# Optimization experiments

Hardware: AMD Instinct MI355X
Metric: run time of the kernel (lower is better)

The kernel has to match this reference:

```python
import jax, jax.numpy as jnp
import numpy as np

MASK_VAL = -10000.0
HEADS = 16

def setup_inputs() -> dict:
    key = jax.random.key(0)
    ks = jax.random.split(key, 4)
    dim = 1024
    x = jax.random.normal(ks[0], (4, 2048, dim), dtype=jnp.float32)
    Wq = jax.random.normal(ks[1], (dim, dim), dtype=jnp.float32) * (dim ** -0.5)
    Wkv = jax.random.normal(ks[2], (dim, 2 * dim), dtype=jnp.float32) * (dim ** -0.5)
    Wout = jax.random.normal(ks[3], (dim, dim), dtype=jnp.float32) * (dim ** -0.5)
    bout = jnp.zeros((dim,), dtype=jnp.float32)
    return {"x": x, "Wq": Wq, "Wkv": Wkv, "Wout": Wout, "bout": bout}

def reference(x, Wq, Wkv, Wout, bout):
    b, n, dim = x.shape
    h = HEADS
    d = dim // h
    scale = dim ** -0.5  # NOTE: module scales by full dim, not head dim
    q = x @ Wq                       # [b,n,dim]
    kv = x @ Wkv                     # [b,n,2*dim]
    k, v = jnp.split(kv, 2, axis=-1)
    split = lambda t: t.reshape(b, n, h, d).transpose(0, 2, 1, 3)  # b h n d
    q, k, v = split(q), split(k), split(v)
    dots = jnp.einsum('bhid,bhjd->bhij', q, k) * scale
    causal = jnp.triu(jnp.ones((n, n), dtype=bool), 1)
    dots = jnp.where(causal, MASK_VAL, dots)
    attn = jax.nn.softmax(dots, axis=-1)
    out = jnp.einsum('bhij,bhjd->bhid', attn, v)
    out = out.transpose(0, 2, 1, 3).reshape(b, n, dim)
    return out @ Wout + bout
```

## Files before the change

kernel.cpp:

```cpp
#include <hip/hip_runtime.h>

typedef unsigned short u16;
typedef __attribute__((ext_vector_type(4))) float f32x4;
typedef __attribute__((ext_vector_type(8))) short bf16x8;

#define MFMA_BF16(a, b, c) __builtin_amdgcn_mfma_f32_16x16x32_bf16((a), (b), (c), 0, 0, 0)

static constexpr int kDim   = 1024;
static constexpr int kSeq   = 2048;
static constexpr int kBatch = 4;
static constexpr int kHeads = 16;
static constexpr int kTok   = kBatch * kSeq;
static constexpr int kQKV   = 3 * kDim;
static constexpr float kQscale = 0.045084220027780106f;

__device__ __forceinline__ u16 f2bf(float f) {
  unsigned int u = __float_as_uint(f);
  u += 0x7fffu + ((u >> 16) & 1u);
  return (u16)(u >> 16);
}

__device__ __forceinline__ float fast_exp2(float x) {
#if __has_builtin(__builtin_amdgcn_exp2f)
  return __builtin_amdgcn_exp2f(x);
#else
  return exp2f(x);
#endif
}

__device__ __forceinline__ unsigned pack_bf16(float lo, float hi) {
  const unsigned ulo = __float_as_uint(lo) + 0x8000u;
  const unsigned uhi = __float_as_uint(hi) + 0x8000u;
#if __has_builtin(__builtin_amdgcn_perm)
  return __builtin_amdgcn_perm(uhi, ulo, 0x07060302u);
#else
  return (uhi & 0xFFFF0000u) | (ulo >> 16);
#endif
}

__device__ __forceinline__ void gl_lds16(const void* g, void* l) {
  __builtin_amdgcn_global_load_lds(
      (const __attribute__((address_space(1))) void*)g,
      (__attribute__((address_space(3))) void*)l, 16, 0, 0);
}

__global__ __launch_bounds__(256) void cvt_f32_to_bf16(const float* __restrict__ in,
                                                       u16* __restrict__ out, int n8) {
  int i = blockIdx.x * 256 + threadIdx.x;
  if (i >= n8) return;
  const float4* p = (const float4*)in + (size_t)i * 2;
  float4 a = p[0], b = p[1];
  alignas(16) u16 o[8];
  o[0] = f2bf(a.x); o[1] = f2bf(a.y); o[2] = f2bf(a.z); o[3] = f2bf(a.w);
  o[4] = f2bf(b.x); o[5] = f2bf(b.y); o[6] = f2bf(b.z); o[7] = f2bf(b.w);
  *(uint4*)(out + (size_t)i * 8) = *(const uint4*)o;
}

__global__ __launch_bounds__(256) void transpose_cvt(const float* __restrict__ src,
                                                     u16* __restrict__ dst, int R, int C) {
  __shared__ u16 tile[64][65];
  const int r0 = blockIdx.y * 64, c0 = blockIdx.x * 64;
  const int t = threadIdx.x;
#pragma unroll
  for (int i = 0; i < 16; ++i) {
    const int idx = i * 256 + t;
    const int rr = idx >> 6, cc = idx & 63;
    tile[rr][cc] = f2bf(src[(size_t)(r0 + rr) * C + c0 + cc]);
  }
  __syncthreads();
#pragma unroll
  for (int i = 0; i < 16; ++i) {
    const int idx = i * 256 + t;
    const int rr = idx >> 6, cc = idx & 63;
    dst[(size_t)(c0 + rr) * R + r0 + cc] = tile[cc][rr];
  }
}

__global__ __launch_bounds__(256) void transpose_v(const u16* __restrict__ QKV,
                                                   u16* __restrict__ Vt) {
  __shared__ u16 tile[64][65];
  const int n0 = blockIdx.x * 64;
  const int bh = blockIdx.y;
  const int b = bh >> 4, h = bh & 15;
  const int t = threadIdx.x;
#pragma unroll
  for (int i = 0; i < 16; ++i) {
    const int idx = i * 256 + t;
    const int nn = idx >> 6, dd = idx & 63;
    tile[nn][dd] = QKV[(size_t)(b * kSeq + n0 + nn) * kQKV + 2048 + h * 64 + dd];
  }
  __syncthreads();
#pragma unroll
  for (int i = 0; i < 16; ++i) {
    const int idx = i * 256 + t;
    const int dd = idx >> 6, nn = idx & 63;
    Vt[((size_t)bh * 64 + dd) * kSeq + n0 + nn] = tile[nn][dd];
  }
}

template <int OUT_F32>
__global__ __launch_bounds__(256) void gemm_bt(const u16* __restrict__ A,
                                               const u16* __restrict__ Bt,
                                               void* __restrict__ Cout,
                                               const float* __restrict__ bias,
                                               int M, int N, int K,
                                               int qcols, float qs) {
  __shared__ u16 As[128 * 32];
  __shared__ u16 Bs[128 * 32];
  const int t = threadIdx.x;
  const int l = t & 63, w = t >> 6;
  const int g = l >> 4, r = l & 15;

  const int gx = gridDim.x;
  int wg = blockIdx.y * gx + blockIdx.x;
  const int chunk = (gx * gridDim.y) >> 3;
  wg = (wg & 7) * chunk + (wg >> 3);
  const int m0 = (wg / gx) * 128, n0 = (wg % gx) * 128;
  const int wr = (w >> 1) * 64, wc = (w & 1) * 64;

  f32x4 acc[4][4];
#pragma unroll
  for (int m = 0; m < 4; ++m)
#pragma unroll
    for (int n = 0; n < 4; ++n) acc[m][n] = f32x4{0.f, 0.f, 0.f, 0.f};

  const int rowi = t >> 2;
  const int coli = (t & 3) * 8;
  const u16* ga = A + (size_t)(m0 + rowi) * K + coli;
  const u16* gb = Bt + (size_t)(n0 + rowi) * K + coli;
  char* lA = (char*)As + t * 16;
  char* lB = (char*)Bs + t * 16;

  for (int k0 = 0; k0 < K; k0 += 32) {
    gl_lds16(ga + k0, lA);
    gl_lds16(ga + k0 + (size_t)64 * K, lA + 4096);
    gl_lds16(gb + k0, lB);
    gl_lds16(gb + k0 + (size_t)64 * K, lB + 4096);
    __syncthreads();
    bf16x8 af[4], bfr[4];
#pragma unroll
    for (int m = 0; m < 4; ++m)
      af[m] = *(const bf16x8*)(As + (wr + m * 16 + r) * 32 + g * 8);
#pragma unroll
    for (int n = 0; n < 4; ++n)
      bfr[n] = *(const bf16x8*)(Bs + (wc + n * 16 + r) * 32 + g * 8);
#pragma unroll
    for (int m = 0; m < 4; ++m)
#pragma unroll
      for (int n = 0; n < 4; ++n)
        acc[m][n] = MFMA_BF16(af[m], bfr[n], acc[m][n]);
    __syncthreads();
  }

#pragma unroll
  for (int m = 0; m < 4; ++m)
#pragma unroll
    for (int n = 0; n < 4; ++n)
#pragma unroll
      for (int j = 0; j < 4; ++j) {
        const int row = m0 + wr + m * 16 + g * 4 + j;
        const int col = n0 + wc + n * 16 + r;
        if (OUT_F32) {
          ((float*)Cout)[(size_t)row * N + col] = acc[m][n][j] + bias[col];
        } else {
          float v = acc[m][n][j];
          if (col < qcols) v *= qs;
          ((u16*)Cout)[(size_t)row * N + col] = f2bf(v);
        }
      }
}

__global__ __launch_bounds__(512, 4) void attn_fwd(const u16* __restrict__ QKV,
                                                   const u16* __restrict__ Vt,
                                                   u16* __restrict__ Ob) {
  __shared__ u16 Kl[64 * 64];
  __shared__ u16 Vl[64 * 64];
  int wg = blockIdx.y * 8 + blockIdx.x;
  wg = (wg & 7) * 64 + (wg >> 3);
  const int ib = wg & 7;
  const int bh = wg >> 3;
  const int b = bh >> 4, h = bh & 15;
  const int t = threadIdx.x;
  const int w = t >> 6;
  const int l = t & 63;
  const int g = l >> 4;
  const int qr = l & 15;
  const int sw = qr & 7;
  const int srow = t >> 3;
  const int sgran = t & 7;
  const int sg_off = (sgran ^ (srow & 7)) * 8;

  const u16* kbase = QKV + (size_t)b * kSeq * kQKV + 1024 + h * 64 + (size_t)srow * kQKV + sg_off;
  const u16* vbase = Vt + ((size_t)bh * 64 + srow) * kSeq + sg_off;

  for (int pass = 0; pass < 2; ++pass) {
    const int qblk = pass ? (15 - ib) : ib;
    const int q0 = qblk * 128;
    const int qrow_g = q0 + w * 16 + qr;

    const u16* qptr = QKV + (size_t)(b * kSeq + qrow_g) * kQKV + h * 64 + g * 8;
    bf16x8 qf[2];
    qf[0] = *(const bf16x8*)qptr;
    qf[1] = *(const bf16x8*)(qptr + 32);

    f32x4 oacc[4];
#pragma unroll
    for (int d = 0; d < 4; ++d) oacc[d] = f32x4{0.f, 0.f, 0.f, 0.f};
    float lsum = 0.f;

    const int nkv = 2 * qblk + 2;
    for (int kb = 0; kb < nkv; ++kb) {
      const int kv0 = kb * 64;
      gl_lds16(kbase + (size_t)kv0 * kQKV, (char*)Kl + t * 16);
      gl_lds16(vbase + kv0, (char*)Vl + t * 16);
      __syncthreads();

      const bool any_valid = kv0 <= q0 + w * 16 + 15;
      const bool need_mask = kv0 + 63 > q0 + w * 16;

      if (any_valid) {
        f32x4 sacc[4];
#pragma unroll
        for (int n = 0; n < 4; ++n) sacc[n] = f32x4{0.f, 0.f, 0.f, 0.f};
        __builtin_amdgcn_s_setprio(1);
#pragma unroll
        for (int n = 0; n < 4; ++n)
#pragma unroll
          for (int c = 0; c < 2; ++c) {
            bf16x8 kf = *(const bf16x8*)(Kl + (n * 16 + qr) * 64 + ((c * 4 + g) ^ sw) * 8);
            sacc[n] = MFMA_BF16(kf, qf[c], sacc[n]);
          }
        __builtin_amdgcn_s_setprio(0);

        float s2[16];
#pragma unroll
        for (int n = 0; n < 4; ++n)
#pragma unroll
          for (int j = 0; j < 4; ++j) s2[n * 4 + j] = sacc[n][j];
        if (need_mask) {
#pragma unroll
          for (int n = 0; n < 4; ++n)
#pragma unroll
            for (int j = 0; j < 4; ++j) {
              const int kv = kv0 + n * 16 + g * 4 + j;
              if (kv > qrow_g) s2[n * 4 + j] = -30000.0f;
            }
        }

        unsigned pk[4][2];
#pragma unroll
        for (int n = 0; n < 4; ++n)
#pragma unroll
          for (int hw = 0; hw < 2; ++hw) {
            const float p0 = fast_exp2(fminf(s2[n * 4 + hw * 2], 60.f));
            const float p1 = fast_exp2(fminf(s2[n * 4 + hw * 2 + 1], 60.f));
            lsum += p0 + p1;
            pk[n][hw] = pack_bf16(p0, p1);
          }

        const int src0 = qr | (((g << 1) & 3) << 4);
        const int src1 = qr | ((((g << 1) + 1) & 3) << 4);
        const bool hi = (g >> 1) != 0;
#pragma unroll
        for (int c = 0; c < 2; ++c) {
          const unsigned a0 = __shfl(pk[2 * c][0], src0);
          const unsigned a1 = __shfl(pk[2 * c][1], src0);
          const unsigned a2 = __shfl(pk[2 * c + 1][0], src0);
          const unsigned a3 = __shfl(pk[2 * c + 1][1], src0);
          const unsigned b0 = __shfl(pk[2 * c][0], src1);
          const unsigned b1 = __shfl(pk[2 * c][1], src1);
          const unsigned b2 = __shfl(pk[2 * c + 1][0], src1);
          const unsigned b3 = __shfl(pk[2 * c + 1][1], src1);
          union { unsigned u[4]; bf16x8 v; } af;
          af.u[0] = hi ? a2 : a0;
          af.u[1] = hi ? a3 : a1;
          af.u[2] = hi ? b2 : b0;
          af.u[3] = hi ? b3 : b1;
          __builtin_amdgcn_s_setprio(1);
#pragma unroll
          for (int d = 0; d < 4; ++d) {
            bf16x8 vf = *(const bf16x8*)(Vl + (d * 16 + qr) * 64 + ((c * 4 + g) ^ sw) * 8);
            oacc[d] = MFMA_BF16(af.v, vf, oacc[d]);
          }
          __builtin_amdgcn_s_setprio(0);
        }
      }
      __syncthreads();
    }

    lsum += __shfl_xor(lsum, 16);
    lsum += __shfl_xor(lsum, 32);
    const float invl = 1.0f / lsum;
    float ir[4];
#pragma unroll
    for (int j = 0; j < 4; ++j) ir[j] = __shfl(invl, (l & 48) | (g * 4 + j));
#pragma unroll
    for (int d = 0; d < 4; ++d)
#pragma unroll
      for (int j = 0; j < 4; ++j) {
        const int row = q0 + w * 16 + g * 4 + j;
        const int col = h * 64 + d * 16 + qr;
        Ob[(size_t)(b * kSeq + row) * kDim + col] = f2bf(oacc[d][j] * ir[j]);
      }
  }
}

extern "C" void kernel_launch(void* const* d_in, const int* in_sizes, int n_in,
                              void* d_out, int out_size, void* d_ws, size_t ws_size,
                              hipStream_t stream) {
  const float* x    = (const float*)d_in[0];
  const float* Wq   = (const float*)d_in[1];
  const float* Wkv  = (const float*)d_in[2];
  const float* Wout = (const float*)d_in[3];
  const float* bout = (const float*)d_in[4];
  float* out = (float*)d_out;

  char* p = (char*)d_ws;
  u16* xb    = (u16*)p; p += (size_t)kTok * kDim * 2;
  u16* Wqkvt = (u16*)p; p += (size_t)kQKV * kDim * 2;
  u16* Wot   = (u16*)p; p += (size_t)kDim * kDim * 2;
  u16* QKV   = (u16*)p; p += (size_t)kTok * kQKV * 2;
  u16* Vt    = (u16*)p; p += (size_t)64 * 64 * kSeq * 2;
  u16* Ob    = (u16*)p; p += (size_t)kTok * kDim * 2;

  const int n8 = kTok * kDim / 8;
  cvt_f32_to_bf16<<<dim3((n8 + 255) / 256), 256, 0, stream>>>(x, xb, n8);
  transpose_cvt<<<dim3(kDim / 64, kDim / 64), 256, 0, stream>>>(Wq, Wqkvt, kDim, kDim);
  transpose_cvt<<<dim3(2 * kDim / 64, kDim / 64), 256, 0, stream>>>(
      Wkv, Wqkvt + (size_t)kDim * kDim, kDim, 2 * kDim);
  transpose_cvt<<<dim3(kDim / 64, kDim / 64), 256, 0, stream>>>(Wout, Wot, kDim, kDim);

  gemm_bt<0><<<dim3(kQKV / 128, kTok / 128), 256, 0, stream>>>(
      xb, Wqkvt, QKV, nullptr, kTok, kQKV, kDim, kDim, kQscale);
  transpose_v<<<dim3(kSeq / 64, kBatch * kHeads), 256, 0, stream>>>(QKV, Vt);
  attn_fwd<<<dim3(kSeq / 256, kBatch * kHeads), 512, 0, stream>>>(QKV, Vt, Ob);
  gemm_bt<1><<<dim3(kDim / 128, kTok / 128), 256, 0, stream>>>(
      Ob, Wot, out, bout, kTok, kDim, kDim, 0, 1.0f);
}
```

Measured before the change: 274.4 us.

## Double-buffer K/V tiles in attention and widen GEMM K-step with swizzled LDS

In the attention kernel, K and V tiles are now double-buffered in shared memory. The next tile's global-to-LDS load is issued before computing on the current one, with explicit vmcnt waits and raw barriers, so load latency overlaps the MFMA and softmax work. In the projection GEMM, the K step grows from 32 to 64 and LDS tiles use an XOR swizzle, which halves the barrier count and is meant to avoid bank conflicts. The cost is double the LDS per block, which may lower occupancy, and a dependence on hand-written waitcnt ordering for correctness.

```diff
diff --git a/kernel.cpp b/kernel.cpp
--- a/kernel.cpp
+++ b/kernel.cpp
@@ -105,8 +105,8 @@
                                                const float* __restrict__ bias,
                                                int M, int N, int K,
                                                int qcols, float qs) {
-  __shared__ u16 As[128 * 32];
-  __shared__ u16 Bs[128 * 32];
+  __shared__ u16 As[128 * 64];
+  __shared__ u16 Bs[128 * 64];
   const int t = threadIdx.x;
   const int l = t & 63, w = t >> 6;
   const int g = l >> 4, r = l & 15;
@@ -124,31 +124,37 @@
 #pragma unroll
     for (int n = 0; n < 4; ++n) acc[m][n] = f32x4{0.f, 0.f, 0.f, 0.f};
 
-  const int rowi = t >> 2;
-  const int coli = (t & 3) * 8;
-  const u16* ga = A + (size_t)(m0 + rowi) * K + coli;
-  const u16* gb = Bt + (size_t)(n0 + rowi) * K + coli;
+  const int srow = t >> 3;
+  const int sgran = t & 7;
+  const int scol = (sgran ^ (srow & 7)) * 8;
+  const u16* ga = A + (size_t)(m0 + srow) * K + scol;
+  const u16* gb = Bt + (size_t)(n0 + srow) * K + scol;
   char* lA = (char*)As + t * 16;
   char* lB = (char*)Bs + t * 16;
-
-  for (int k0 = 0; k0 < K; k0 += 32) {
-    gl_lds16(ga + k0, lA);
-    gl_lds16(ga + k0 + (size_t)64 * K, lA + 4096);
-    gl_lds16(gb + k0, lB);
-    gl_lds16(gb + k0 + (size_t)64 * K, lB + 4096);
+  const int rsw = r & 7;
+
+  for (int k0 = 0; k0 < K; k0 += 64) {
+#pragma unroll
+    for (int i = 0; i < 4; ++i) {
+      gl_lds16(ga + k0 + (size_t)(i * 32) * K, lA + i * 4096);
+      gl_lds16(gb + k0 + (size_t)(i * 32) * K, lB + i * 4096);
+    }
     __syncthreads();
-    bf16x8 af[4], bfr[4];
-#pragma unroll
-    for (int m = 0; m < 4; ++m)
-      af[m] = *(const bf16x8*)(As + (wr + m * 16 + r) * 32 + g * 8);
-#pragma unroll
-    for (int n = 0; n < 4; ++n)
-      bfr[n] = *(const bf16x8*)(Bs + (wc + n * 16 + r) * 32 + g * 8);
-#pragma unroll
-    for (int m = 0; m < 4; ++m)
+#pragma unroll
+    for (int kk = 0; kk < 2; ++kk) {
+      bf16x8 af[4], bfr[4];
+#pragma unroll
+      for (int m = 0; m < 4; ++m)
+        af[m] = *(const bf16x8*)(As + (wr + m * 16 + r) * 64 + (((kk * 4 + g) ^ rsw) * 8));
 #pragma unroll
       for (int n = 0; n < 4; ++n)
-        acc[m][n] = MFMA_BF16(af[m], bfr[n], acc[m][n]);
+        bfr[n] = *(const bf16x8*)(Bs + (wc + n * 16 + r) * 64 + (((kk * 4 + g) ^ rsw) * 8));
+#pragma unroll
+      for (int m = 0; m < 4; ++m)
+#pragma unroll
+        for (int n = 0; n < 4; ++n)
+          acc[m][n] = MFMA_BF16(af[m], bfr[n], acc[m][n]);
+    }
     __syncthreads();
   }
 
@@ -173,8 +179,8 @@
 __global__ __launch_bounds__(512, 4) void attn_fwd(const u16* __restrict__ QKV,
                                                    const u16* __restrict__ Vt,
                                                    u16* __restrict__ Ob) {
-  __shared__ u16 Kl[64 * 64];
-  __shared__ u16 Vl[64 * 64];
+  __shared__ u16 Kl[2][64 * 64];
+  __shared__ u16 Vl[2][64 * 64];
   int wg = blockIdx.y * 8 + blockIdx.x;
   wg = (wg & 7) * 64 + (wg >> 3);
   const int ib = wg & 7;
@@ -209,12 +215,26 @@
     float lsum = 0.f;
 
     const int nkv = 2 * qblk + 2;
+
+    gl_lds16(kbase, (char*)Kl[0] + t * 16);
+    gl_lds16(vbase, (char*)Vl[0] + t * 16);
+
     for (int kb = 0; kb < nkv; ++kb) {
+      const int cur = kb & 1;
+      if (kb + 1 < nkv) {
+        const int kv1 = (kb + 1) * 64;
+        gl_lds16(kbase + (size_t)kv1 * kQKV, (char*)Kl[cur ^ 1] + t * 16);
+        gl_lds16(vbase + kv1, (char*)Vl[cur ^ 1] + t * 16);
+        asm volatile("s_waitcnt vmcnt(2)" ::: "memory");
+      } else {
+        asm volatile("s_waitcnt vmcnt(0)" ::: "memory");
+      }
+      __builtin_amdgcn_s_barrier();
+      __builtin_amdgcn_sched_barrier(0);
+
+      const u16* Kc = Kl[cur];
+      const u16* Vc = Vl[cur];
       const int kv0 = kb * 64;
-      gl_lds16(kbase + (size_t)kv0 * kQKV, (char*)Kl + t * 16);
-      gl_lds16(vbase + kv0, (char*)Vl + t * 16);
-      __syncthreads();
-
       const bool any_valid = kv0 <= q0 + w * 16 + 15;
       const bool need_mask = kv0 + 63 > q0 + w * 16;
 
@@ -227,7 +247,7 @@
         for (int n = 0; n < 4; ++n)
 #pragma unroll
           for (int c = 0; c < 2; ++c) {
-            bf16x8 kf = *(const bf16x8*)(Kl + (n * 16 + qr) * 64 + ((c * 4 + g) ^ sw) * 8);
+            bf16x8 kf = *(const bf16x8*)(Kc + (n * 16 + qr) * 64 + ((c * 4 + g) ^ sw) * 8);
             sacc[n] = MFMA_BF16(kf, qf[c], sacc[n]);
           }
         __builtin_amdgcn_s_setprio(0);
@@ -279,13 +299,13 @@
           __builtin_amdgcn_s_setprio(1);
 #pragma unroll
           for (int d = 0; d < 4; ++d) {
-            bf16x8 vf = *(const bf16x8*)(Vl + (d * 16 + qr) * 64 + ((c * 4 + g) ^ sw) * 8);
+            bf16x8 vf = *(const bf16x8*)(Vc + (d * 16 + qr) * 64 + ((c * 4 + g) ^ sw) * 8);
             oacc[d] = MFMA_BF16(af.v, vf, oacc[d]);
           }
           __builtin_amdgcn_s_setprio(0);
         }
       }
-      __syncthreads();
+      __builtin_amdgcn_s_barrier();
     }
 
     lsum += __shfl_xor(lsum, 16);
```

Measured after the change: 261.9 us. 1.05x faster.
